# Optimization experiments

Measured on AMD Instinct MI355X. Metric: run time of the kernel, lower is better.

Reference implementation:

```python
import jax, jax.numpy as jnp
import numpy as np

MARGIN = 0.1  # init kwarg: margin
# type_of_distance='euclidean', type_of_quadruplets='hard', what_is_hard='one'


def _distance_euclidean(x):
    # l2-normalize rows, then all-pairs euclidean distance (torch.cdist p=2)
    x = x / jnp.linalg.norm(x, axis=1, keepdims=True)
    sq = jnp.sum(x * x, axis=1)
    d2 = sq[:, None] + sq[None, :] - 2.0 * (x @ x.T)
    return jnp.sqrt(jnp.maximum(d2, 0.0))


def setup_inputs() -> dict:
    key = jax.random.key(0)
    k1, k2 = jax.random.split(key)
    B, D, C = 256, 512, 80
    logits = jax.random.normal(k1, (B, D), dtype=jnp.float32)
    # sparse multi-hot labels: ~2.4 active classes per sample
    labels = (jax.random.uniform(k2, (B, C)) < 0.03).astype(jnp.float32)
    return {"logits": logits, "labels": labels}


def reference(logits, labels):
    n = labels.shape[0]
    sames = (labels @ labels.T) > 0                      # [B,B] bool
    diffs = ~sames
    sames = sames & ~jnp.eye(n, dtype=bool)              # fill_diagonal_(0)
    triu = jnp.triu(jnp.ones((n, n), dtype=bool), k=1)   # J < K
    # O(B^3) quadruplet-candidate mask: sames[I,J] & sames[I,K] & (J<K)
    mask = sames[:, :, None] & sames[:, None, :] & triu[None, :, :]
    I, J, K = jnp.nonzero(mask)                          # row-major, same as torch.where
    # expand each (I,J,K) triplet with every negative N of anchor I
    rows, cols = jnp.nonzero(diffs[I])                   # [n_quads]
    quadruplets = jnp.stack([I[rows], J[rows], K[rows], cols], axis=1)

    mat = _distance_euclidean(jax.lax.stop_gradient(logits))  # logits.detach()
    Ii, Jj, Kk, Nn = quadruplets[:, 0], quadruplets[:, 1], quadruplets[:, 2], quadruplets[:, 3]
    ij = mat[Ii, Jj]
    ik = mat[Ii, Kk]
    innd = mat[Ii, Nn]
    m1 = innd - ij
    m2 = innd - ik
    # type_of_quadruplets='hard', what_is_hard='one' (opt = OR)
    cond = ((m1 <= MARGIN) | (m2 <= MARGIN)) & ((m1 <= 0) | (m2 <= 0))
    return quadruplets[cond]
```

## Files before the change

kernel.cpp:

```cpp
#include <hip/hip_runtime.h>
#include <math.h>

#define NB 256
#define ND 512
#define NC 80
#define NSPLIT 8
#define SLOT 32640

__device__ float g_x [NB * ND];
__device__ float g_xt[ND * NB];
__device__ float g_sq[NB];
__device__ float g_ddneg[NB * NB];
__device__ unsigned long long g_m[NB * 2];
__device__ int   g_atot[NB];
__device__ int   g_T[NB];
__device__ int4  g_trip[NB * SLOT];

__device__ __forceinline__ int block_scan(int val, int* tmp) {
    int tid = threadIdx.x;
    __syncthreads();
    tmp[tid] = val;
    __syncthreads();
    #pragma unroll
    for (int off = 1; off < 256; off <<= 1) {
        int v = (tid >= off) ? tmp[tid - off] : 0;
        __syncthreads();
        tmp[tid] += v;
        __syncthreads();
    }
    return tmp[tid];
}

__device__ __forceinline__ int ubcount(const float* s, float thr) {
    int pos = 0;
    #pragma unroll
    for (int step = 128; step > 0; step >>= 1) {
        int np = pos + step;
        if (s[np - 1] <= thr) pos = np;
    }
    return pos;
}

__global__ __launch_bounds__(256) void k_prep(const float* __restrict__ logits,
                                              const float* __restrict__ labels) {
    int b = blockIdx.x, tid = threadIdx.x;
    __shared__ double red[NB];
    float v0 = logits[b * ND + tid];
    float v1 = logits[b * ND + 256 + tid];
    red[tid] = (double)(v0 * v0) + (double)(v1 * v1);
    __syncthreads();
    for (int off = 128; off > 0; off >>= 1) {
        if (tid < off) red[tid] += red[tid + off];
        __syncthreads();
    }
    float S = (float)red[0];
    float nrm = sqrtf(S);
    __syncthreads();
    float a0 = v0 / nrm;
    float a1 = v1 / nrm;
    g_x[b * ND + tid]          = a0;
    g_x[b * ND + 256 + tid]    = a1;
    g_xt[tid * NB + b]         = a0;
    g_xt[(tid + 256) * NB + b] = a1;
    red[tid] = (double)(a0 * a0) + (double)(a1 * a1);
    __syncthreads();
    for (int off = 128; off > 0; off >>= 1) {
        if (tid < off) red[tid] += red[tid + off];
        __syncthreads();
    }
    if (tid == 0) g_sq[b] = (float)red[0];
    int wv = tid >> 6, ln = tid & 63;
    if (wv == 0) {
        unsigned long long m0 = __ballot(labels[b * NC + ln] != 0.0f);
        if (ln == 0) g_m[2 * b] = m0;
    } else if (wv == 1) {
        bool p = (ln < 16) ? (labels[b * NC + 64 + ln] != 0.0f) : false;
        unsigned long long m1 = __ballot(p);
        if (ln == 0) g_m[2 * b + 1] = m1;
    }
}

__global__ __launch_bounds__(256) void k_count() {
    __shared__ float xi[ND];
    __shared__ float s_dd[NB], s_ddneg[NB], s_sort[NB];
    __shared__ int s_tmp[NB], s_rowbase[NB];
    __shared__ short s_plist[NB];
    int i = blockIdx.x, tid = threadIdx.x;
    xi[tid]       = g_x[i * ND + tid];
    xi[tid + 256] = g_x[i * ND + 256 + tid];
    __syncthreads();
    double dot = 0.0;
    #pragma unroll 8
    for (int c = 0; c < ND; ++c)
        dot = fma((double)xi[c], (double)g_xt[c * NB + tid], dot);
    float dotf = (float)dot;
    float sm   = g_sq[i] + g_sq[tid];
    float d2   = sm - 2.0f * dotf;
    float dv   = sqrtf(d2 > 0.0f ? d2 : 0.0f);
    s_dd[tid] = dv;
    unsigned long long mi0 = g_m[2 * i],   mi1 = g_m[2 * i + 1];
    unsigned long long mt0 = g_m[2 * tid], mt1 = g_m[2 * tid + 1];
    bool shl   = ((mi0 & mt0) | (mi1 & mt1)) != 0ULL;
    bool isPos = shl && (tid != i);
    float ddneg = shl ? INFINITY : dv;
    s_ddneg[tid] = ddneg;
    g_ddneg[i * NB + tid] = ddneg;
    int incl = block_scan(isPos ? 1 : 0, s_tmp);
    int P = s_tmp[255];
    if (isPos) s_plist[incl - 1] = (short)tid;
    if (tid < P - 1) s_rowbase[tid] = tid * (P - 1) - (tid * (tid - 1)) / 2;
    s_sort[tid] = s_ddneg[tid];
    __syncthreads();
    for (int k = 2; k <= 256; k <<= 1)
        for (int j = k >> 1; j > 0; j >>= 1) {
            int p = tid ^ j;
            float mine = s_sort[tid], oth = s_sort[p];
            bool keepmin = (((tid & k) == 0) == (tid < p));
            float res = keepmin ? fminf(mine, oth) : fmaxf(mine, oth);
            __syncthreads();
            s_sort[tid] = res;
            __syncthreads();
        }
    int T = P * (P - 1) / 2;
    if (tid == 0) g_T[i] = T;
    int carried = 0;
    for (int cb = 0; cb < T; cb += NB) {
        int t = cb + tid;
        int cnt = 0, jk = 0;
        float thr = 0.0f;
        if (t < T) {
            int a = 0;
            #pragma unroll
            for (int step = 128; step > 0; step >>= 1) {
                int na = a + step;
                if (na <= P - 2 && s_rowbase[na] <= t) a = na;
            }
            int b = a + 1 + (t - s_rowbase[a]);
            int jj = s_plist[a], kk = s_plist[b];
            thr = fmaxf(s_dd[jj], s_dd[kk]);
            jk  = jj | (kk << 8);
            cnt = ubcount(s_sort, thr);
        }
        int inc2 = block_scan(cnt, s_tmp);
        if (t < T)
            g_trip[i * SLOT + t] =
                make_int4(jk, __float_as_int(thr), carried + inc2 - cnt, 0);
        carried += s_tmp[255];
    }
    if (tid == 0) g_atot[i] = carried;
}

__global__ __launch_bounds__(256) void k_write(int4* __restrict__ out, int maxQuads) {
    __shared__ int s_tmp[NB];
    int i = blockIdx.x / NSPLIT;
    int split = blockIdx.x % NSPLIT;
    int tid = threadIdx.x;
    int wv = tid >> 6, ln = tid & 63;
    block_scan(g_atot[tid], s_tmp);
    int anchorBase = s_tmp[i] - g_atot[i];
    float vneg[4];
    #pragma unroll
    for (int r = 0; r < 4; ++r) vneg[r] = g_ddneg[i * NB + ((r << 6) | ln)];
    int T = g_T[i];
    int waveId = (split << 2) | wv;
    for (int t = waveId; t < T; t += NSPLIT * 4) {
        int4 tr = g_trip[i * SLOT + t];
        int jj = tr.x & 255, kk = tr.x >> 8;
        float thr = __int_as_float(tr.y);
        int base = anchorBase + tr.z;
        int cum = 0;
        #pragma unroll
        for (int r = 0; r < 4; ++r) {
            bool flag = (vneg[r] <= thr);
            unsigned long long mask = __ballot(flag);
            if (flag) {
                int pos = base + cum + __popcll(mask & ((1ULL << ln) - 1ULL));
                if (pos < maxQuads) out[pos] = make_int4(i, jj, kk, (r << 6) | ln);
            }
            cum += __popcll(mask);
        }
    }
}

extern "C" void kernel_launch(void* const* d_in, const int* in_sizes, int n_in,
                              void* d_out, int out_size, void* d_ws, size_t ws_size,
                              hipStream_t stream) {
    const float* logits = (const float*)d_in[0];
    const float* labels = (const float*)d_in[1];
    if (n_in >= 2 && in_sizes[0] == NB * NC && in_sizes[1] == NB * ND) {
        logits = (const float*)d_in[1];
        labels = (const float*)d_in[0];
    }
    int maxQuads = out_size / 4;

    k_prep <<<NB, NB, 0, stream>>>(logits, labels);
    k_count<<<NB, NB, 0, stream>>>();
    k_write<<<NB * NSPLIT, NB, 0, stream>>>((int4*)d_out, maxQuads);
}
```

Baseline: 196.1 us.

## Use wave shuffles in bitonic sort and simplify write-kernel prefix and loads

The bitonic sort in k_count keeps each value in a register and uses wavefront xor-shuffles for strides below 64. It only falls back to shared memory with barriers for larger strides, which removes most of the per-step __syncthreads. k_write replaces the block-wide scan for the anchor base with a single-wave strided sum plus shuffle reduction, and it prefetches the next triplet record. Its four ballots are also issued together before the stores. Together these cut barrier overhead and hide the triplet load latency, at the cost of more register pressure.

Result: faster. 191.7 us (-2.2%).

```diff
diff --git a/kernel.cpp b/kernel.cpp
--- a/kernel.cpp
+++ b/kernel.cpp
@@ -109,18 +109,24 @@
     int P = s_tmp[255];
     if (isPos) s_plist[incl - 1] = (short)tid;
     if (tid < P - 1) s_rowbase[tid] = tid * (P - 1) - (tid * (tid - 1)) / 2;
-    s_sort[tid] = s_ddneg[tid];
-    __syncthreads();
+    float v = ddneg;
     for (int k = 2; k <= 256; k <<= 1)
         for (int j = k >> 1; j > 0; j >>= 1) {
-            int p = tid ^ j;
-            float mine = s_sort[tid], oth = s_sort[p];
-            bool keepmin = (((tid & k) == 0) == (tid < p));
-            float res = keepmin ? fminf(mine, oth) : fmaxf(mine, oth);
-            __syncthreads();
-            s_sort[tid] = res;
-            __syncthreads();
+            float oth;
+            if (j >= 64) {
+                __syncthreads();
+                s_sort[tid] = v;
+                __syncthreads();
+                oth = s_sort[tid ^ j];
+            } else {
+                oth = __shfl_xor(v, j);
+            }
+            bool keepmin = (((tid & k) == 0) == ((tid & j) == 0));
+            v = keepmin ? fminf(v, oth) : fmaxf(v, oth);
         }
+    __syncthreads();
+    s_sort[tid] = v;
+    __syncthreads();
     int T = P * (P - 1) / 2;
     if (tid == 0) g_T[i] = T;
     int carried = 0;
@@ -151,34 +157,46 @@
 }
 
 __global__ __launch_bounds__(256) void k_write(int4* __restrict__ out, int maxQuads) {
-    __shared__ int s_tmp[NB];
     int i = blockIdx.x / NSPLIT;
     int split = blockIdx.x % NSPLIT;
     int tid = threadIdx.x;
     int wv = tid >> 6, ln = tid & 63;
-    block_scan(g_atot[tid], s_tmp);
-    int anchorBase = s_tmp[i] - g_atot[i];
+    int psum = 0;
+    for (int m = ln; m < i; m += 64) psum += g_atot[m];
+    #pragma unroll
+    for (int off = 1; off < 64; off <<= 1) psum += __shfl_xor(psum, off);
+    int anchorBase = psum;
     float vneg[4];
     #pragma unroll
     for (int r = 0; r < 4; ++r) vneg[r] = g_ddneg[i * NB + ((r << 6) | ln)];
+    unsigned long long lanemask = (1ULL << ln) - 1ULL;
     int T = g_T[i];
     int waveId = (split << 2) | wv;
-    for (int t = waveId; t < T; t += NSPLIT * 4) {
-        int4 tr = g_trip[i * SLOT + t];
+    int t = waveId;
+    int4 tr = (t < T) ? g_trip[i * SLOT + t] : make_int4(0, 0, 0, 0);
+    while (t < T) {
+        int tn = t + NSPLIT * 4;
+        int4 nxt = (tn < T) ? g_trip[i * SLOT + tn] : make_int4(0, 0, 0, 0);
         int jj = tr.x & 255, kk = tr.x >> 8;
         float thr = __int_as_float(tr.y);
         int base = anchorBase + tr.z;
-        int cum = 0;
-        #pragma unroll
-        for (int r = 0; r < 4; ++r) {
-            bool flag = (vneg[r] <= thr);
-            unsigned long long mask = __ballot(flag);
-            if (flag) {
-                int pos = base + cum + __popcll(mask & ((1ULL << ln) - 1ULL));
-                if (pos < maxQuads) out[pos] = make_int4(i, jj, kk, (r << 6) | ln);
-            }
-            cum += __popcll(mask);
-        }
+        bool f0 = (vneg[0] <= thr), f1 = (vneg[1] <= thr);
+        bool f2 = (vneg[2] <= thr), f3 = (vneg[3] <= thr);
+        unsigned long long m0 = __ballot(f0), m1 = __ballot(f1);
+        unsigned long long m2 = __ballot(f2), m3 = __ballot(f3);
+        int b1 = base + __popcll(m0);
+        int b2 = b1 + __popcll(m1);
+        int b3 = b2 + __popcll(m2);
+        if (f0) { int pos = base + __popcll(m0 & lanemask);
+                  if (pos < maxQuads) out[pos] = make_int4(i, jj, kk, ln); }
+        if (f1) { int pos = b1 + __popcll(m1 & lanemask);
+                  if (pos < maxQuads) out[pos] = make_int4(i, jj, kk, 64 | ln); }
+        if (f2) { int pos = b2 + __popcll(m2 & lanemask);
+                  if (pos < maxQuads) out[pos] = make_int4(i, jj, kk, 128 | ln); }
+        if (f3) { int pos = b3 + __popcll(m3 & lanemask);
+                  if (pos < maxQuads) out[pos] = make_int4(i, jj, kk, 192 | ln); }
+        tr = nxt;
+        t = tn;
     }
 }
 
```
